# Kernel tuning notes

Hardware: AMD Instinct MI355X
Metric: run time of the kernel (lower is better)

## Reference

```python
import jax, jax.numpy as jnp
import numpy as np

EPS = 1e-6
H, A, V = 4, 64, 64  # heads, attn_dim, hidden_dim


def layer_norm(x, w, b):
    mu = jnp.mean(x, axis=-1, keepdims=True)
    var = jnp.var(x, axis=-1, keepdims=True)
    return (x - mu) * jax.lax.rsqrt(var + EPS) * w + b


def setup_inputs() -> dict:
    key = jax.random.key(0)
    B, N, D = 4, 2048, 512
    lengths = np.array([2048, 1536, 1024, 1792], np.int32)
    offsets = np.concatenate([[0], np.cumsum(lengths)]).astype(np.int32)
    L = int(offsets[-1])  # 6400
    uvqk_out = (2 * V + 2 * A) * H  # 1024
    out_in = 2 * V * H + D          # concat([u, x, normed_attn])
    ks = jax.random.split(key, 4)
    return {
        "x": jax.random.normal(ks[0], (L, D), jnp.float32),
        "x_lengths": jnp.asarray(lengths),
        "x_offsets": jnp.asarray(offsets),
        "max_seq_len": N,
        "num_targets": jnp.asarray([32, 16, 8, 64], jnp.int32),
        "uvqk_weight": jax.random.normal(ks[1], (D, uvqk_out), jnp.float32) / np.float32(np.sqrt(D)),
        "uvqk_bias": jnp.zeros((uvqk_out,), jnp.float32),
        "input_norm_weight": jnp.ones((D,), jnp.float32),
        "input_norm_bias": jnp.zeros((D,), jnp.float32),
        "output_norm_weight": jnp.ones((V * H,), jnp.float32),
        "output_norm_bias": jnp.zeros((V * H,), jnp.float32),
        "output_weight": jax.random.normal(ks[2], (out_in, D), jnp.float32) / np.float32(np.sqrt(out_in)),
    }


def reference(x, x_lengths, x_offsets, max_seq_len, num_targets,
              uvqk_weight, uvqk_bias, input_norm_weight, input_norm_bias,
              output_norm_weight, output_norm_bias, output_weight):
    L, D = x.shape
    B = x_lengths.shape[0]
    N = int(max_seq_len)
    alpha = A ** -0.5

    # fused input layernorm + UVQK projection + silu
    nx = layer_norm(x, input_norm_weight, input_norm_bias)
    uvqk = jax.nn.silu(nx @ uvqk_weight + uvqk_bias)              # [L, (2V+2A)*H]
    u = uvqk[:, : V * H]                                          # [L, V*H]
    v = uvqk[:, V * H: 2 * V * H].reshape(L, H, V)
    q = uvqk[:, 2 * V * H: 2 * V * H + A * H].reshape(L, H, A)
    k = uvqk[:, 2 * V * H + A * H:].reshape(L, H, A)

    # jagged -> padded [B, N, ...]
    pos = jnp.arange(N)
    gather_idx = jnp.clip(x_offsets[:-1, None] + pos[None, :], 0, L - 1)  # [B,N]
    valid = pos[None, :] < x_lengths[:, None]                              # [B,N]
    qp = q[gather_idx] * valid[..., None, None]
    kp = k[gather_idx] * valid[..., None, None]
    vp = v[gather_idx] * valid[..., None, None]

    # target-aware causal mask: clamp ids at uih boundary; eye | dist>0
    max_ids = (x_lengths - num_targets)[:, None]        # [B,1]
    ids = jnp.minimum(pos[None, :], max_ids)            # [B,N]
    dist = ids[:, :, None] - ids[:, None, :]            # [B,N,N]
    mask = (dist > 0) | jnp.eye(N, dtype=bool)[None]
    mask = mask & valid[:, :, None] & valid[:, None, :]

    scores = jnp.einsum("bnha,bmha->bhnm", qp, kp) * alpha
    attn_w = jax.nn.silu(scores) * (1.0 / N)
    attn_w = attn_w * mask[:, None].astype(attn_w.dtype)
    attn_p = jnp.einsum("bhnm,bmhv->bnhv", attn_w, vp).reshape(B, N, H * V)

    # padded -> jagged
    tok = jnp.arange(L)
    b_of = jnp.searchsorted(x_offsets, tok, side="right") - 1
    p_of = tok - x_offsets[b_of]
    attn = attn_p[b_of, p_of]                            # [L, H*V]

    # output: norm(attn), concat [u, x, y], project, residual (dropout off / eval)
    y = layer_norm(attn, output_norm_weight, output_norm_bias)
    y = jnp.concatenate([u, x, y], axis=1)
    return x + y @ output_weight
```

## Files before the change

### kernel.cpp

```cpp
#include <hip/hip_runtime.h>
#include <math.h>

#define NSEQ 2048
#define PIT 72

typedef __attribute__((ext_vector_type(8))) short short8;
typedef __attribute__((ext_vector_type(4))) short short4v;
typedef __attribute__((ext_vector_type(4))) float f32x4;

__device__ __forceinline__ float silu_f(float z) {
    return z * __builtin_amdgcn_rcpf(1.f + __expf(-z));
}

__device__ __forceinline__ unsigned short f2bf(float f) {
    unsigned int u = __float_as_uint(f);
    u += 0x7fffu + ((u >> 16) & 1u);
    return (unsigned short)(u >> 16);
}

__device__ __forceinline__ unsigned short f2bf_fast(float f) {
    return (unsigned short)((__float_as_uint(f) + 0x8000u) >> 16);
}

__device__ __forceinline__ short8 scale8_pow2(short8 v, float s) {
    short8 r;
    #pragma unroll
    for (int i = 0; i < 8; i++) {
        float f = __uint_as_float(((unsigned int)(unsigned short)v[i]) << 16) * s;
        r[i] = (short)(unsigned short)(__float_as_uint(f) >> 16);
    }
    return r;
}

__global__ void __launch_bounds__(256) transpose_to_bf16(
    const float* __restrict__ W, unsigned short* __restrict__ Wt, int R, int C)
{
    __shared__ float t[32][33];
    int tid = threadIdx.x;
    int tr = tid >> 5, tc = tid & 31;
    int r0 = blockIdx.y * 32, c0 = blockIdx.x * 32;
    #pragma unroll
    for (int p = 0; p < 4; p++)
        t[tr + p * 8][tc] = W[(size_t)(r0 + tr + p * 8) * C + c0 + tc];
    __syncthreads();
    #pragma unroll
    for (int p = 0; p < 4; p++)
        Wt[(size_t)(c0 + tr + p * 8) * R + r0 + tc] = f2bf(t[tc][tr + p * 8]);
}

__global__ void __launch_bounds__(256) ln512_kernel(
    const float* __restrict__ x, const float* __restrict__ w,
    const float* __restrict__ b,
    unsigned short* __restrict__ nxb, unsigned short* __restrict__ A2)
{
    int tid = threadIdx.x;
    int r = tid >> 7;
    int row = blockIdx.x * 2 + r;
    int c = (tid & 127) * 4;
    float4 v = *(const float4*)(x + (size_t)row * 512 + c);
    float s = v.x + v.y + v.z + v.w;
    float sq = v.x * v.x + v.y * v.y + v.z * v.z + v.w * v.w;
    for (int o = 32; o > 0; o >>= 1) { s += __shfl_down(s, o); sq += __shfl_down(sq, o); }
    __shared__ float red[8];
    int wv = tid >> 6;
    if ((tid & 63) == 0) { red[wv] = s; red[4 + wv] = sq; }
    __syncthreads();
    float ts = red[2 * r] + red[2 * r + 1];
    float tq = red[4 + 2 * r] + red[4 + 2 * r + 1];
    float mu = ts * (1.f / 512.f);
    float var = tq * (1.f / 512.f) - mu * mu;
    float rs = rsqrtf(var + 1e-6f);
    float4 wv4 = *(const float4*)(w + c);
    float4 bv4 = *(const float4*)(b + c);
    ushort4 hn, hx;
    hn.x = f2bf((v.x - mu) * rs * wv4.x + bv4.x);
    hn.y = f2bf((v.y - mu) * rs * wv4.y + bv4.y);
    hn.z = f2bf((v.z - mu) * rs * wv4.z + bv4.z);
    hn.w = f2bf((v.w - mu) * rs * wv4.w + bv4.w);
    hx.x = f2bf(v.x); hx.y = f2bf(v.y); hx.z = f2bf(v.z); hx.w = f2bf(v.w);
    *(ushort4*)(nxb + (size_t)row * 512 + c) = hn;
    *(ushort4*)(A2 + (size_t)row * 1024 + 256 + c) = hx;
}

__global__ void __launch_bounds__(256) ln256_kernel(
    const float* __restrict__ a, const float* __restrict__ w,
    const float* __restrict__ b, unsigned short* __restrict__ A2)
{
    int tid = threadIdx.x;
    int r = tid >> 7;
    int row = blockIdx.x * 2 + r;
    int c = (tid & 127) * 2;
    float2 v = *(const float2*)(a + (size_t)row * 256 + c);
    float s = v.x + v.y, sq = v.x * v.x + v.y * v.y;
    for (int o = 32; o > 0; o >>= 1) { s += __shfl_down(s, o); sq += __shfl_down(sq, o); }
    __shared__ float red[8];
    int wv = tid >> 6;
    if ((tid & 63) == 0) { red[wv] = s; red[4 + wv] = sq; }
    __syncthreads();
    float ts = red[2 * r] + red[2 * r + 1];
    float tq = red[4 + 2 * r] + red[4 + 2 * r + 1];
    float mu = ts * (1.f / 256.f);
    float var = tq * (1.f / 256.f) - mu * mu;
    float rs = rsqrtf(var + 1e-6f);
    float2 w2 = *(const float2*)(w + c);
    float2 b2 = *(const float2*)(b + c);
    ushort2 h;
    h.x = f2bf((v.x - mu) * rs * w2.x + b2.x);
    h.y = f2bf((v.y - mu) * rs * w2.y + b2.y);
    *(ushort2*)(A2 + (size_t)row * 1024 + 768 + c) = h;
}

__global__ void __launch_bounds__(256) gemm1_mfma(
    const unsigned short* __restrict__ Ab, const unsigned short* __restrict__ Bt,
    const float* __restrict__ bias,
    unsigned short* __restrict__ A2, unsigned short* __restrict__ qkvb)
{
    constexpr int K = 512, KIT = K / 64;
    __shared__ unsigned short As[64 * PIT];
    __shared__ unsigned short Bs[128 * PIT];
    int tid = threadIdx.x, lane = tid & 63, w = tid >> 6;
    int wr = w >> 1, wc = w & 1;
    int nn = lane & 15, qd = lane >> 4;
    int bm = blockIdx.y * 64, bn = blockIdx.x * 128;
    int arow = tid >> 2, ac0 = (tid & 3) * 16;
    int brow = tid >> 1, bc0 = (tid & 1) * 32;
    const unsigned short* Ag = Ab + (size_t)(bm + arow) * K + ac0;
    const unsigned short* Bg = Bt + (size_t)(bn + brow) * K + bc0;

    short8 pa0 = *(const short8*)Ag, pa1 = *(const short8*)(Ag + 8);
    short8 pb0 = *(const short8*)Bg, pb1 = *(const short8*)(Bg + 8);
    short8 pb2 = *(const short8*)(Bg + 16), pb3 = *(const short8*)(Bg + 24);

    f32x4 acc[2][4];
    #pragma unroll
    for (int i = 0; i < 2; i++)
        #pragma unroll
        for (int j = 0; j < 4; j++) acc[i][j] = (f32x4){0.f, 0.f, 0.f, 0.f};

    for (int it = 0; it < KIT; ++it) {
        __syncthreads();
        *(short8*)&As[arow * PIT + ac0]     = pa0;
        *(short8*)&As[arow * PIT + ac0 + 8] = pa1;
        *(short8*)&Bs[brow * PIT + bc0]      = pb0;
        *(short8*)&Bs[brow * PIT + bc0 + 8]  = pb1;
        *(short8*)&Bs[brow * PIT + bc0 + 16] = pb2;
        *(short8*)&Bs[brow * PIT + bc0 + 24] = pb3;
        __syncthreads();
        if (it + 1 < KIT) {
            int k0 = (it + 1) * 64;
            pa0 = *(const short8*)(Ag + k0); pa1 = *(const short8*)(Ag + k0 + 8);
            pb0 = *(const short8*)(Bg + k0); pb1 = *(const short8*)(Bg + k0 + 8);
            pb2 = *(const short8*)(Bg + k0 + 16); pb3 = *(const short8*)(Bg + k0 + 24);
        }
        #pragma unroll
        for (int kk = 0; kk < 2; kk++) {
            short8 af[2], bf[4];
            #pragma unroll
            for (int i = 0; i < 2; i++)
                af[i] = *(const short8*)&As[(wr * 32 + i * 16 + nn) * PIT + kk * 32 + qd * 8];
            #pragma unroll
            for (int j = 0; j < 4; j++)
                bf[j] = *(const short8*)&Bs[(wc * 64 + j * 16 + nn) * PIT + kk * 32 + qd * 8];
            #pragma unroll
            for (int i = 0; i < 2; i++)
                #pragma unroll
                for (int j = 0; j < 4; j++)
                    acc[i][j] = __builtin_amdgcn_mfma_f32_16x16x32_bf16(af[i], bf[j], acc[i][j], 0, 0, 0);
        }
    }
    bool isU = (bn < 256);
    #pragma unroll
    for (int j = 0; j < 4; j++) {
        int col = bn + wc * 64 + j * 16 + nn;
        float bb = bias[col];
        #pragma unroll
        for (int i = 0; i < 2; i++) {
            int rbase = bm + wr * 32 + i * 16 + qd * 4;
            #pragma unroll
            for (int r = 0; r < 4; r++) {
                unsigned short hh = f2bf(silu_f(acc[i][j][r] + bb));
                if (isU) A2[(size_t)(rbase + r) * 1024 + col] = hh;
                else     qkvb[(size_t)(rbase + r) * 768 + col - 256] = hh;
            }
        }
    }
}

__global__ void __launch_bounds__(256) gemm2_mfma(
    const unsigned short* __restrict__ Ab, const unsigned short* __restrict__ Bt,
    const float* __restrict__ x, float* __restrict__ out)
{
    constexpr int K = 1024, KIT = K / 64;
    __shared__ unsigned short As[64 * PIT];
    __shared__ unsigned short Bs[128 * PIT];
    int tid = threadIdx.x, lane = tid & 63, w = tid >> 6;
    int wr = w >> 1, wc = w & 1;
    int nn = lane & 15, qd = lane >> 4;
    int bm = blockIdx.y * 64, bn = blockIdx.x * 128;
    int arow = tid >> 2, ac0 = (tid & 3) * 16;
    int brow = tid >> 1, bc0 = (tid & 1) * 32;
    const unsigned short* Ag = Ab + (size_t)(bm + arow) * K + ac0;
    const unsigned short* Bg = Bt + (size_t)(bn + brow) * K + bc0;

    short8 pa0 = *(const short8*)Ag, pa1 = *(const short8*)(Ag + 8);
    short8 pb0 = *(const short8*)Bg, pb1 = *(const short8*)(Bg + 8);
    short8 pb2 = *(const short8*)(Bg + 16), pb3 = *(const short8*)(Bg + 24);

    f32x4 acc[2][4];
    #pragma unroll
    for (int i = 0; i < 2; i++)
        #pragma unroll
        for (int j = 0; j < 4; j++) acc[i][j] = (f32x4){0.f, 0.f, 0.f, 0.f};

    for (int it = 0; it < KIT; ++it) {
        __syncthreads();
        *(short8*)&As[arow * PIT + ac0]     = pa0;
        *(short8*)&As[arow * PIT + ac0 + 8] = pa1;
        *(short8*)&Bs[brow * PIT + bc0]      = pb0;
        *(short8*)&Bs[brow * PIT + bc0 + 8]  = pb1;
        *(short8*)&Bs[brow * PIT + bc0 + 16] = pb2;
        *(short8*)&Bs[brow * PIT + bc0 + 24] = pb3;
        __syncthreads();
        if (it + 1 < KIT) {
            int k0 = (it + 1) * 64;
            pa0 = *(const short8*)(Ag + k0); pa1 = *(const short8*)(Ag + k0 + 8);
            pb0 = *(const short8*)(Bg + k0); pb1 = *(const short8*)(Bg + k0 + 8);
            pb2 = *(const short8*)(Bg + k0 + 16); pb3 = *(const short8*)(Bg + k0 + 24);
        }
        #pragma unroll
        for (int kk = 0; kk < 2; kk++) {
            short8 af[2], bf[4];
            #pragma unroll
            for (int i = 0; i < 2; i++)
                af[i] = *(const short8*)&As[(wr * 32 + i * 16 + nn) * PIT + kk * 32 + qd * 8];
            #pragma unroll
            for (int j = 0; j < 4; j++)
                bf[j] = *(const short8*)&Bs[(wc * 64 + j * 16 + nn) * PIT + kk * 32 + qd * 8];
            #pragma unroll
            for (int i = 0; i < 2; i++)
                #pragma unroll
                for (int j = 0; j < 4; j++)
                    acc[i][j] = __builtin_amdgcn_mfma_f32_16x16x32_bf16(af[i], bf[j], acc[i][j], 0, 0, 0);
        }
    }
    #pragma unroll
    for (int j = 0; j < 4; j++) {
        int col = bn + wc * 64 + j * 16 + nn;
        #pragma unroll
        for (int i = 0; i < 2; i++) {
            int rbase = bm + wr * 32 + i * 16 + qd * 4;
            #pragma unroll
            for (int r = 0; r < 4; r++) {
                size_t idx = (size_t)(rbase + r) * 512 + col;
                out[idx] = x[idx] + acc[i][j][r];
            }
        }
    }
}

__global__ void __launch_bounds__(256, 2) attn_mfma_kernel(
    const unsigned short* __restrict__ qkvb,
    const int* __restrict__ offsets,
    const int* __restrict__ lengths,
    const int* __restrict__ num_targets,
    float* __restrict__ attn)
{
    int bh = blockIdx.y;
    int b = bh >> 2, h = bh & 3;
    int len = lengths[b];
    int n0 = (31 - (int)blockIdx.x) * 64;
    if (n0 >= len) return;
    int m_hi = min(n0 + 63, len - 1);
    int off = offsets[b];
    int max_id = len - num_targets[b];
    int tid = threadIdx.x, lane = tid & 63, w = tid >> 6;
    int nn = lane & 15, qd = lane >> 4;

    __shared__ __align__(16) char smem[69632];
    unsigned short* Vt = (unsigned short*)(smem + w * 9216);
    float* Os = (float*)smem;

    short8 qf[4][2];
    #pragma unroll
    for (int g = 0; g < 4; g++) {
        int row = min(n0 + g * 16 + nn, len - 1);
        const unsigned short* base = qkvb + (size_t)(off + row) * 768 + 256 + h * 64;
        qf[g][0] = scale8_pow2(*(const short8*)(base + qd * 8), 0.125f);
        qf[g][1] = scale8_pow2(*(const short8*)(base + 32 + qd * 8), 0.125f);
    }

    f32x4 o_acc[4][4];
    #pragma unroll
    for (int t = 0; t < 4; t++)
        #pragma unroll
        for (int g = 0; g < 4; g++) o_acc[t][g] = (f32x4){0.f, 0.f, 0.f, 0.f};

    int fast_lim = min(n0, max_id);
    int r0 = (lane & 15) * 4, d0 = (lane >> 4) * 16;

    short8 kf[4][2], kn[4][2], vf[4][2];
    int m_first = w * 64;
    if (m_first <= m_hi) {
        #pragma unroll
        for (int s = 0; s < 4; s++) {
            int row = min(m_first + s * 16 + nn, len - 1);
            const unsigned short* kb = qkvb + (size_t)(off + row) * 768 + 512 + h * 64 + qd * 8;
            kf[s][0] = *(const short8*)kb;
            kf[s][1] = *(const short8*)(kb + 32);
        }
        #pragma unroll
        for (int j = 0; j < 4; j++) {
            int row = min(m_first + r0 + j, len - 1);
            const unsigned short* vb = qkvb + (size_t)(off + row) * 768 + h * 64 + d0;
            vf[j][0] = *(const short8*)vb;
            vf[j][1] = *(const short8*)(vb + 8);
        }
    }

    for (int m0 = m_first; m0 <= m_hi; m0 += 256) {
        #pragma unroll
        for (int dd = 0; dd < 16; dd++) {
            int hh = dd >> 3, e = dd & 7;
            short4v pk;
            pk[0] = vf[0][hh][e]; pk[1] = vf[1][hh][e];
            pk[2] = vf[2][hh][e]; pk[3] = vf[3][hh][e];
            *(short4v*)&Vt[(d0 + dd) * PIT + r0] = pk;
        }
        int mnext = m0 + 256;
        if (mnext <= m_hi) {
            #pragma unroll
            for (int j = 0; j < 4; j++) {
                int row = min(mnext + r0 + j, len - 1);
                const unsigned short* vb = qkvb + (size_t)(off + row) * 768 + h * 64 + d0;
                vf[j][0] = *(const short8*)vb;
                vf[j][1] = *(const short8*)(vb + 8);
            }
            #pragma unroll
            for (int s = 0; s < 4; s++) {
                int row = min(mnext + s * 16 + nn, len - 1);
                const unsigned short* kb = qkvb + (size_t)(off + row) * 768 + 512 + h * 64 + qd * 8;
                kn[s][0] = *(const short8*)kb;
                kn[s][1] = *(const short8*)(kb + 32);
            }
        }
        bool fastp = (m0 + 63 < fast_lim);
        #pragma unroll
        for (int s = 0; s < 4; s++) {
            f32x4 st[4];
            #pragma unroll
            for (int g = 0; g < 4; g++) {
                st[g] = (f32x4){0.f, 0.f, 0.f, 0.f};
                st[g] = __builtin_amdgcn_mfma_f32_16x16x32_bf16(kf[s][0], qf[g][0], st[g], 0, 0, 0);
                st[g] = __builtin_amdgcn_mfma_f32_16x16x32_bf16(kf[s][1], qf[g][1], st[g], 0, 0, 0);
            }
            short4v bop[4];
            if (fastp) {
                #pragma unroll
                for (int g = 0; g < 4; g++)
                    #pragma unroll
                    for (int r = 0; r < 4; r++)
                        bop[g][r] = (short)f2bf_fast(silu_f(st[g][r]));
            } else {
                #pragma unroll
                for (int g = 0; g < 4; g++) {
                    int nc_ = n0 + g * 16 + nn;
                    int id_ = min(nc_, max_id);
                    #pragma unroll
                    for (int r = 0; r < 4; r++) {
                        int mcol = m0 + s * 16 + qd * 4 + r;
                        bool ok = (mcol < id_) || (mcol == nc_);
                        bop[g][r] = (short)f2bf_fast(ok ? silu_f(st[g][r]) : 0.f);
                    }
                }
            }
            #pragma unroll
            for (int t = 0; t < 4; t++) {
                short4v aop = *(const short4v*)&Vt[(t * 16 + nn) * PIT + s * 16 + qd * 4];
                #pragma unroll
                for (int g = 0; g < 4; g++)
                    o_acc[t][g] = __builtin_amdgcn_mfma_f32_16x16x16bf16_1k(aop, bop[g], o_acc[t][g], 0, 0, 0);
            }
        }
        if (mnext <= m_hi) {
            #pragma unroll
            for (int s = 0; s < 4; s++) { kf[s][0] = kn[s][0]; kf[s][1] = kn[s][1]; }
        }
    }

    __syncthreads();
    const float invN = 1.f / (float)NSEQ;
    float* Ow = Os + w * 4352;
    #pragma unroll
    for (int t = 0; t < 4; t++)
        #pragma unroll
        for (int g = 0; g < 4; g++) {
            f32x4 v = o_acc[t][g] * invN;
            *(f32x4*)&Ow[(g * 16 + nn) * 68 + t * 16 + qd * 4] = v;
        }
    __syncthreads();
    int rr = tid >> 2, cs = (tid & 3) * 16;
    if (n0 + rr < len) {
        float* dst = attn + (size_t)(off + n0 + rr) * 256 + h * 64 + cs;
        #pragma unroll
        for (int q4 = 0; q4 < 4; q4++) {
            f32x4 v = (f32x4){0.f, 0.f, 0.f, 0.f};
            #pragma unroll
            for (int w2 = 0; w2 < 4; w2++)
                v += *(const f32x4*)&Os[w2 * 4352 + rr * 68 + cs + q4 * 4];
            *(f32x4*)(dst + q4 * 4) = v;
        }
    }
}

extern "C" void kernel_launch(void* const* d_in, const int* in_sizes, int n_in,
                              void* d_out, int out_size, void* d_ws, size_t ws_size,
                              hipStream_t stream)
{
    const float* x          = (const float*)d_in[0];
    const int*   x_lengths  = (const int*)d_in[1];
    const int*   x_offsets  = (const int*)d_in[2];
    const int*   num_targets = (const int*)d_in[4];
    const float* uvqk_w     = (const float*)d_in[5];
    const float* uvqk_b     = (const float*)d_in[6];
    const float* in_w       = (const float*)d_in[7];
    const float* in_b       = (const float*)d_in[8];
    const float* out_w      = (const float*)d_in[9];
    const float* out_b      = (const float*)d_in[10];
    const float* Wo         = (const float*)d_in[11];
    float* out = (float*)d_out;

    int L = in_sizes[0] / 512;
    int B = in_sizes[1];

    char* ws = (char*)d_ws;
    size_t o = 0;
    float* attn = (float*)(ws + o);          o += (size_t)L * 256 * 4;
    unsigned short* nxb  = (unsigned short*)(ws + o); o += (size_t)L * 512 * 2;
    unsigned short* A2   = (unsigned short*)(ws + o); o += (size_t)L * 1024 * 2;
    unsigned short* qkvb = (unsigned short*)(ws + o); o += (size_t)L * 768 * 2;
    unsigned short* W1t  = (unsigned short*)(ws + o); o += (size_t)1024 * 512 * 2;
    unsigned short* W2t  = (unsigned short*)(ws + o); o += (size_t)512 * 1024 * 2;

    transpose_to_bf16<<<dim3(1024 / 32, 512 / 32), 256, 0, stream>>>(uvqk_w, W1t, 512, 1024);
    transpose_to_bf16<<<dim3(512 / 32, 1024 / 32), 256, 0, stream>>>(Wo, W2t, 1024, 512);

    ln512_kernel<<<L / 2, 256, 0, stream>>>(x, in_w, in_b, nxb, A2);

    dim3 g1(1024 / 128, L / 64);
    gemm1_mfma<<<g1, 256, 0, stream>>>(nxb, W1t, uvqk_b, A2, qkvb);

    dim3 g2(NSEQ / 64, 16);
    attn_mfma_kernel<<<g2, 256, 0, stream>>>(qkvb, x_offsets, x_lengths, num_targets, attn);

    ln256_kernel<<<L / 2, 256, 0, stream>>>(attn, out_w, out_b, A2);

    dim3 g3(512 / 128, L / 64);
    gemm2_mfma<<<g3, 256, 0, stream>>>(A2, W2t, x, out);
}
```

Before: 170.7 us.

## Split attention key range across two blocks with atomic accumulation

The attention kernel's key dimension is split over two blocks (grid x=2), each covering alternating 256-key chunks with stride 512. Partial outputs are combined into the attn buffer with float atomicAdd, which is zeroed by a memset. The in-block reduction now uses two LDS buffers instead of four, cutting shared memory from 69,632 to 36,864 bytes so more blocks can be resident. The aim is more parallelism and better load balance for long causal rows, at the cost of an extra memset, atomic traffic, and nondeterministic summation order.

```diff
diff --git a/kernel.cpp b/kernel.cpp
--- a/kernel.cpp
+++ b/kernel.cpp
@@ -265,20 +265,24 @@
     const int* __restrict__ num_targets,
     float* __restrict__ attn)
 {
-    int bh = blockIdx.y;
+    int bh = blockIdx.z;
     int b = bh >> 2, h = bh & 3;
     int len = lengths[b];
-    int n0 = (31 - (int)blockIdx.x) * 64;
+    int n0 = (31 - (int)blockIdx.y) * 64;
     if (n0 >= len) return;
     int m_hi = min(n0 + 63, len - 1);
+    int s = (int)blockIdx.x;
+    if (s == 1 && m_hi < 256) return;
     int off = offsets[b];
     int max_id = len - num_targets[b];
     int tid = threadIdx.x, lane = tid & 63, w = tid >> 6;
     int nn = lane & 15, qd = lane >> 4;
-
-    __shared__ __align__(16) char smem[69632];
+    int ws8 = s * 4 + w;
+
+    __shared__ __align__(16) char smem[36864];
     unsigned short* Vt = (unsigned short*)(smem + w * 9216);
-    float* Os = (float*)smem;
+    float* OsA = (float*)smem;
+    float* OsB = (float*)(smem + 17408);
 
     short8 qf[4][2];
     #pragma unroll
@@ -299,14 +303,14 @@
     int r0 = (lane & 15) * 4, d0 = (lane >> 4) * 16;
 
     short8 kf[4][2], kn[4][2], vf[4][2];
-    int m_first = w * 64;
+    int m_first = ws8 * 64;
     if (m_first <= m_hi) {
         #pragma unroll
-        for (int s = 0; s < 4; s++) {
-            int row = min(m_first + s * 16 + nn, len - 1);
+        for (int ss = 0; ss < 4; ss++) {
+            int row = min(m_first + ss * 16 + nn, len - 1);
             const unsigned short* kb = qkvb + (size_t)(off + row) * 768 + 512 + h * 64 + qd * 8;
-            kf[s][0] = *(const short8*)kb;
-            kf[s][1] = *(const short8*)(kb + 32);
+            kf[ss][0] = *(const short8*)kb;
+            kf[ss][1] = *(const short8*)(kb + 32);
         }
         #pragma unroll
         for (int j = 0; j < 4; j++) {
@@ -317,7 +321,7 @@
         }
     }
 
-    for (int m0 = m_first; m0 <= m_hi; m0 += 256) {
+    for (int m0 = m_first; m0 <= m_hi; m0 += 512) {
         #pragma unroll
         for (int dd = 0; dd < 16; dd++) {
             int hh = dd >> 3, e = dd & 7;
@@ -326,7 +330,7 @@
             pk[2] = vf[2][hh][e]; pk[3] = vf[3][hh][e];
             *(short4v*)&Vt[(d0 + dd) * PIT + r0] = pk;
         }
-        int mnext = m0 + 256;
+        int mnext = m0 + 512;
         if (mnext <= m_hi) {
             #pragma unroll
             for (int j = 0; j < 4; j++) {
@@ -336,22 +340,22 @@
                 vf[j][1] = *(const short8*)(vb + 8);
             }
             #pragma unroll
-            for (int s = 0; s < 4; s++) {
-                int row = min(mnext + s * 16 + nn, len - 1);
+            for (int ss = 0; ss < 4; ss++) {
+                int row = min(mnext + ss * 16 + nn, len - 1);
                 const unsigned short* kb = qkvb + (size_t)(off + row) * 768 + 512 + h * 64 + qd * 8;
-                kn[s][0] = *(const short8*)kb;
-                kn[s][1] = *(const short8*)(kb + 32);
+                kn[ss][0] = *(const short8*)kb;
+                kn[ss][1] = *(const short8*)(kb + 32);
             }
         }
         bool fastp = (m0 + 63 < fast_lim);
         #pragma unroll
-        for (int s = 0; s < 4; s++) {
+        for (int ss = 0; ss < 4; ss++) {
             f32x4 st[4];
             #pragma unroll
             for (int g = 0; g < 4; g++) {
                 st[g] = (f32x4){0.f, 0.f, 0.f, 0.f};
-                st[g] = __builtin_amdgcn_mfma_f32_16x16x32_bf16(kf[s][0], qf[g][0], st[g], 0, 0, 0);
-                st[g] = __builtin_amdgcn_mfma_f32_16x16x32_bf16(kf[s][1], qf[g][1], st[g], 0, 0, 0);
+                st[g] = __builtin_amdgcn_mfma_f32_16x16x32_bf16(kf[ss][0], qf[g][0], st[g], 0, 0, 0);
+                st[g] = __builtin_amdgcn_mfma_f32_16x16x32_bf16(kf[ss][1], qf[g][1], st[g], 0, 0, 0);
             }
             short4v bop[4];
             if (fastp) {
@@ -367,7 +371,7 @@
                     int id_ = min(nc_, max_id);
                     #pragma unroll
                     for (int r = 0; r < 4; r++) {
-                        int mcol = m0 + s * 16 + qd * 4 + r;
+                        int mcol = m0 + ss * 16 + qd * 4 + r;
                         bool ok = (mcol < id_) || (mcol == nc_);
                         bop[g][r] = (short)f2bf_fast(ok ? silu_f(st[g][r]) : 0.f);
                     }
@@ -375,7 +379,7 @@
             }
             #pragma unroll
             for (int t = 0; t < 4; t++) {
-                short4v aop = *(const short4v*)&Vt[(t * 16 + nn) * PIT + s * 16 + qd * 4];
+                short4v aop = *(const short4v*)&Vt[(t * 16 + nn) * PIT + ss * 16 + qd * 4];
                 #pragma unroll
                 for (int g = 0; g < 4; g++)
                     o_acc[t][g] = __builtin_amdgcn_mfma_f32_16x16x16bf16_1k(aop, bop[g], o_acc[t][g], 0, 0, 0);
@@ -383,31 +387,43 @@
         }
         if (mnext <= m_hi) {
             #pragma unroll
-            for (int s = 0; s < 4; s++) { kf[s][0] = kn[s][0]; kf[s][1] = kn[s][1]; }
-        }
-    }
-
-    __syncthreads();
+            for (int ss = 0; ss < 4; ss++) { kf[ss][0] = kn[ss][0]; kf[ss][1] = kn[ss][1]; }
+        }
+    }
+
     const float invN = 1.f / (float)NSEQ;
-    float* Ow = Os + w * 4352;
-    #pragma unroll
-    for (int t = 0; t < 4; t++)
-        #pragma unroll
-        for (int g = 0; g < 4; g++) {
-            f32x4 v = o_acc[t][g] * invN;
-            *(f32x4*)&Ow[(g * 16 + nn) * 68 + t * 16 + qd * 4] = v;
-        }
+    __syncthreads();
+    if (w < 2) {
+        float* Ow = (w == 0) ? OsA : OsB;
+        #pragma unroll
+        for (int t = 0; t < 4; t++)
+            #pragma unroll
+            for (int g = 0; g < 4; g++)
+                *(f32x4*)&Ow[(g * 16 + nn) * 68 + t * 16 + qd * 4] = o_acc[t][g] * invN;
+    }
+    __syncthreads();
+    if (w >= 2) {
+        float* Ow = (w == 2) ? OsA : OsB;
+        #pragma unroll
+        for (int t = 0; t < 4; t++)
+            #pragma unroll
+            for (int g = 0; g < 4; g++) {
+                float* p = &Ow[(g * 16 + nn) * 68 + t * 16 + qd * 4];
+                f32x4 cur = *(f32x4*)p;
+                *(f32x4*)p = cur + o_acc[t][g] * invN;
+            }
+    }
     __syncthreads();
     int rr = tid >> 2, cs = (tid & 3) * 16;
     if (n0 + rr < len) {
         float* dst = attn + (size_t)(off + n0 + rr) * 256 + h * 64 + cs;
         #pragma unroll
         for (int q4 = 0; q4 < 4; q4++) {
-            f32x4 v = (f32x4){0.f, 0.f, 0.f, 0.f};
-            #pragma unroll
-            for (int w2 = 0; w2 < 4; w2++)
-                v += *(const f32x4*)&Os[w2 * 4352 + rr * 68 + cs + q4 * 4];
-            *(f32x4*)(dst + q4 * 4) = v;
+            f32x4 v = *(const f32x4*)&OsA[rr * 68 + cs + q4 * 4];
+            v += *(const f32x4*)&OsB[rr * 68 + cs + q4 * 4];
+            #pragma unroll
+            for (int e = 0; e < 4; e++)
+                atomicAdd(dst + q4 * 4 + e, v[e]);
         }
     }
 }
@@ -441,6 +457,8 @@
     unsigned short* W1t  = (unsigned short*)(ws + o); o += (size_t)1024 * 512 * 2;
     unsigned short* W2t  = (unsigned short*)(ws + o); o += (size_t)512 * 1024 * 2;
 
+    hipMemsetAsync(attn, 0, (size_t)L * 256 * 4, stream);
+
     transpose_to_bf16<<<dim3(1024 / 32, 512 / 32), 256, 0, stream>>>(uvqk_w, W1t, 512, 1024);
     transpose_to_bf16<<<dim3(512 / 32, 1024 / 32), 256, 0, stream>>>(Wo, W2t, 1024, 512);
 
@@ -449,7 +467,7 @@
     dim3 g1(1024 / 128, L / 64);
     gemm1_mfma<<<g1, 256, 0, stream>>>(nxb, W1t, uvqk_b, A2, qkvb);
 
-    dim3 g2(NSEQ / 64, 16);
+    dim3 g2(2, NSEQ / 64, 16);
     attn_mfma_kernel<<<g2, 256, 0, stream>>>(qkvb, x_offsets, x_lengths, num_targets, attn);
 
     ln256_kernel<<<L / 2, 256, 0, stream>>>(attn, out_w, out_b, A2);
```

Result: slower. 292.1 us (+71.2%).
